# Optimization experiments

Measured on AMD Instinct MI355X. Metric: run time of the kernel, lower is better.

Reference implementation:

```python
import jax, jax.numpy as jnp
import numpy as np

CH = 512
COND = 1280
HEADS = 8
GROUPS = CH // 8
EPS = 1e-5


def conv2d(x, w, b, pad):
    y = jax.lax.conv_general_dilated(
        x, w, window_strides=(1, 1), padding=[(pad, pad), (pad, pad)],
        dimension_numbers=('NCHW', 'OIHW', 'NCHW'))
    return y + b[None, :, None, None]


def group_norm(x, gamma, beta, groups, eps=EPS):
    b, c, h, w = x.shape
    xg = x.reshape(b, groups, c // groups, h, w)
    mu = xg.mean(axis=(2, 3, 4), keepdims=True)
    var = xg.var(axis=(2, 3, 4), keepdims=True)
    xn = ((xg - mu) * jax.lax.rsqrt(var + eps)).reshape(b, c, h, w)
    return xn * gamma[None, :, None, None] + beta[None, :, None, None]


def setup_inputs() -> dict:
    key = jax.random.key(0)
    ks = jax.random.split(key, 20)
    s = 0.05
    inp = {
        'x': jax.random.normal(ks[0], (8, CH, 32, 32), jnp.float32),
        'conditioning': jax.random.normal(ks[1], (8, COND), jnp.float32),
        # ResBlock params
        'c1w': jax.random.normal(ks[2], (CH, CH, 3, 3), jnp.float32) * s,
        'c1b': jnp.zeros((CH,), jnp.float32),
        'g1w': jnp.ones((CH,), jnp.float32),
        'g1b': jnp.zeros((CH,), jnp.float32),
        'c2w': jax.random.normal(ks[3], (CH, CH, 3, 3), jnp.float32) * s,
        'c2b': jnp.zeros((CH,), jnp.float32),
        'g2w': jnp.ones((CH,), jnp.float32),
        'g2b': jnp.zeros((CH,), jnp.float32),
        'cpw': jax.random.normal(ks[4], (CH, COND), jnp.float32) * s,
        'cpb': jnp.zeros((CH,), jnp.float32),
        'rpw': jax.random.normal(ks[5], (CH, CH, 1, 1), jnp.float32) * s,
        'rpb': jnp.zeros((CH,), jnp.float32),
        # Attention params (1x1 convs)
        'qw': jax.random.normal(ks[6], (CH, CH, 1, 1), jnp.float32) * s,
        'qb': jnp.zeros((CH,), jnp.float32),
        'kw': jax.random.normal(ks[7], (CH, CH, 1, 1), jnp.float32) * s,
        'kb': jnp.zeros((CH,), jnp.float32),
        'vw': jax.random.normal(ks[8], (CH, CH, 1, 1), jnp.float32) * s,
        'vb': jnp.zeros((CH,), jnp.float32),
        'ow': jax.random.normal(ks[9], (CH, CH, 1, 1), jnp.float32) * s,
        'ob': jnp.zeros((CH,), jnp.float32),
    }
    return inp


def reference(x, conditioning, c1w, c1b, g1w, g1b, c2w, c2b, g2w, g2b,
              cpw, cpb, rpw, rpb, qw, qb, kw, kb, vw, vb, ow, ob):
    # --- ResBlock ---
    residual = conv2d(x, rpw, rpb, 0)
    h = conv2d(x, c1w, c1b, 1)
    h = group_norm(h, g1w, g1b, GROUPS)
    h = jax.nn.silu(h)
    h = conv2d(h, c2w, c2b, 1)
    h = group_norm(h, g2w, g2b, GROUPS)
    cond = conditioning @ cpw.T + cpb  # [B, C]
    h = h * (1.0 + cond[:, :, None, None]) + residual

    # --- SpatialSelfAttention ---
    b, c, hh, ww = h.shape
    d = c // HEADS
    scale = d ** (-0.5)
    q = conv2d(h, qw, qb, 0).reshape(b, HEADS, d, hh * ww)
    k = conv2d(h, kw, kb, 0).reshape(b, HEADS, d, hh * ww)
    v = conv2d(h, vw, vb, 0).reshape(b, HEADS, d, hh * ww)
    attn = jnp.einsum('bhdn,bhdm->bhnm', q, k) * scale  # [B,H,N,N]
    attn = jax.nn.softmax(attn, axis=-1)
    out = jnp.einsum('bhnm,bhdm->bhdn', attn, v).reshape(b, c, hh, ww)
    return conv2d(out, ow, ob, 0) + h
```

## Files before the change

### kernel.cpp

```cpp
#include <hip/hip_runtime.h>
#include <hip/hip_bf16.h>

typedef unsigned short u16;
typedef unsigned long long u64;
typedef __attribute__((ext_vector_type(8))) short bf8;
typedef __attribute__((ext_vector_type(4))) short bf4;
typedef __attribute__((ext_vector_type(4))) float f32x4;

#define CH_ 512
#define NSP 1024
#define NB 8
#define CONDDIM 1280
#define NGROUP 64
#define HEADS_ 8
#define HD 64
#define PR 34
#define PPB (PR*PR)
#define QSCALE 0.18033688011112042f

#define VWAIT(N) asm volatile("s_waitcnt vmcnt(" #N ")" ::: "memory")
#define SCHEDB __builtin_amdgcn_sched_barrier(0)
#define BARRIER do { SCHEDB; __builtin_amdgcn_s_barrier(); SCHEDB; } while (0)

__device__ __forceinline__ u16 f2bf(float f) {
  union { float f; unsigned u; } v; v.f = f;
  unsigned u = v.u;
  return (u16)((u + 0x7fffu + ((u >> 16) & 1u)) >> 16);
}

__device__ __forceinline__ unsigned cvt_pk_bf16(float lo, float hi) {
  unsigned r;
  asm volatile("v_cvt_pk_bf16_f32 %0, %1, %2" : "=v"(r) : "v"(lo), "v"(hi));
  return r;
}

__device__ __forceinline__ f32x4 mfma_bf16(bf8 a, bf8 b, f32x4 c) {
  return __builtin_amdgcn_mfma_f32_16x16x32_bf16(a, b, c, 0, 0, 0);
}

__device__ __forceinline__ void gload16(const void* g, void* l) {
  __builtin_amdgcn_global_load_lds((const __attribute__((address_space(1))) void*)g,
                                   (__attribute__((address_space(3))) void*)l, 16, 0, 0);
}


__global__ __launch_bounds__(1024) void pack_x_kernel(const float* __restrict__ x, u16* __restrict__ xp) {
  __shared__ float t[32][33];
  int b = blockIdx.z;
  int c0 = blockIdx.y * 32, p0 = blockIdx.x * 32;
  int tx = threadIdx.x & 31, ty = threadIdx.x >> 5;
  t[ty][tx] = x[((size_t)b * CH_ + c0 + ty) * NSP + p0 + tx];
  __syncthreads();
  int p = p0 + ty;
  int y = p >> 5, xc = p & 31;
  xp[((size_t)b * PPB + (size_t)(y + 1) * PR + xc + 1) * CH_ + c0 + tx] = f2bf(t[tx][ty]);
}

__global__ __launch_bounds__(256) void border_zero_kernel(u16* __restrict__ a, u16* __restrict__ b) {
  int id = blockIdx.x * 256 + threadIdx.x;
  if (id >= NB * 132 * 64) return;
  int ch8 = id & 63;
  int rest = id >> 6;
  int bidx = rest % 132;
  int bb = rest / 132;
  int r, c;
  if (bidx < 34)       { r = 0;          c = bidx; }
  else if (bidx < 68)  { r = 33;         c = bidx - 34; }
  else if (bidx < 100) { r = bidx - 67;  c = 0; }
  else                 { r = bidx - 99;  c = 33; }
  size_t off = ((size_t)bb * PPB + (size_t)r * PR + c) * CH_ + ch8 * 8;
  const bf8 z = {0, 0, 0, 0, 0, 0, 0, 0};
  *(bf8*)(a + off) = z;
  *(bf8*)(b + off) = z;
}

__global__ __launch_bounds__(256) void pack_w3_kernel(const float* __restrict__ wA, const float* __restrict__ wB,
                                                      u16* __restrict__ dA, u16* __restrict__ dB) {
  int id = blockIdx.x * 256 + threadIdx.x;
  if (id >= 9 * 64 * CH_) return;
  const float* w = blockIdx.y ? wB : wA;
  u16* wp = blockIdx.y ? dB : dA;
  int co = id & (CH_ - 1);
  int cib = (id >> 9) & 63;
  int t = id >> 15;
  int dy = t / 3, dx = t % 3;
  bf8 v;
#pragma unroll
  for (int j = 0; j < 8; j++) {
    int ci = cib * 8 + j;
    v[j] = (short)f2bf(w[(((size_t)co * CH_ + ci) * 3 + dy) * 3 + dx]);
  }
  *(bf8*)(wp + ((size_t)(t * 64 + cib) * CH_ + co) * 8) = v;
}

__global__ __launch_bounds__(256) void pack_w1_kernel(
    const float* __restrict__ s0, const float* __restrict__ s1, const float* __restrict__ s2,
    const float* __restrict__ s3, const float* __restrict__ s4,
    u16* __restrict__ d0, u16* __restrict__ d1, u16* __restrict__ d2,
    u16* __restrict__ d3, u16* __restrict__ d4) {
  int id = blockIdx.x * 256 + threadIdx.x;
  if (id >= 64 * CH_) return;
  const float* w; u16* wp;
  switch (blockIdx.y) {
    case 0: w = s0; wp = d0; break;
    case 1: w = s1; wp = d1; break;
    case 2: w = s2; wp = d2; break;
    case 3: w = s3; wp = d3; break;
    default: w = s4; wp = d4; break;
  }
  int co = id & (CH_ - 1);
  int cib = id >> 9;
  bf8 v;
#pragma unroll
  for (int j = 0; j < 8; j++) v[j] = (short)f2bf(w[(size_t)co * CH_ + cib * 8 + j]);
  *(bf8*)(wp + ((size_t)cib * CH_ + co) * 8) = v;
}

__global__ __launch_bounds__(256) void cond_kernel(const float* __restrict__ cd, const float* __restrict__ cpw,
                                                   const float* __restrict__ cpb, float* __restrict__ cond) {
  int b = blockIdx.y;
  int c = blockIdx.x * 4 + (threadIdx.x >> 6);
  int lane = threadIdx.x & 63;
  const float* wrow = cpw + (size_t)c * CONDDIM;
  const float* crow = cd + (size_t)b * CONDDIM;
  float s = 0.f;
  for (int i = lane; i < CONDDIM; i += 64) s += crow[i] * wrow[i];
#pragma unroll
  for (int m = 32; m > 0; m >>= 1) s += __shfl_xor(s, m, 64);
  if (lane == 0) cond[b * CH_ + c] = s + cpb[c];
}

template <int TAPS, int PIN, int EPI>
__global__ __launch_bounds__(256, 3) void conv_kernel(
    const u16* __restrict__ in, const u16* __restrict__ wp, const float* __restrict__ bias,
    float* __restrict__ outf, const float* __restrict__ addf,
    u16* __restrict__ o0, u16* __restrict__ o1, u16* __restrict__ o2,
    const float* __restrict__ b0, const float* __restrict__ b1, const float* __restrict__ b2) {
  constexpr int LDSZ = (TAPS == 9) ? (2 * 14336 + 2 * 12288) : (4 * 8192 + 4 * 4096);
  __shared__ char lds[LDSZ];
  char* ldsA = lds;
  char* ldsB = lds + ((TAPS == 9) ? 2 * 14336 : 4 * 8192);

  const int b = blockIdx.z;
  int seg = 0, coy = blockIdx.y;
  if constexpr (EPI == 5) { seg = coy >> 3; coy &= 7; }
  const int co0 = coy * 64;
  const int p0 = blockIdx.x * 128;
  const int tid = threadIdx.x;
  const int lane = tid & 63, wid = tid >> 6;
  const int wv = wid >> 1, wc = wid & 1;
  const int l15 = lane & 15, lhi = lane >> 4;

  const char* aSrc;
  if constexpr (TAPS == 9) {
    aSrc = (const char*)in + ((size_t)b * PPB + (size_t)blockIdx.x * 4 * PR) * 1024;
  } else if constexpr (PIN) {
    aSrc = (const char*)in + (size_t)b * PPB * 1024;
  } else {
    aSrc = (const char*)in + ((size_t)b * NSP + p0) * 1024;
  }
  const char* bSrc = (const char*)wp + (size_t)((EPI == 5) ? seg * 524288 : 0) + co0 * 16;

  const int pB = ((tid >> 6) * 512 + (tid & 63)) * 16;
  int pA0, pA1, pA3 = 0;
  if constexpr (TAPS == 9) {
    pA0 = ((tid >> 2) << 10) + ((tid & 3) << 4);
    pA3 = ((192 + ((tid & 127) >> 2)) << 10) + ((tid & 3) << 4);
    pA1 = 0;
  } else {
    int a0 = (tid >> 2), a1 = 64 + (tid >> 2);
    if constexpr (PIN) {
      int pp0 = p0 + a0, pp1 = p0 + a1;
      int g0 = ((pp0 >> 5) + 1) * PR + (pp0 & 31) + 1;
      int g1 = ((pp1 >> 5) + 1) * PR + (pp1 & 31) + 1;
      pA0 = (g0 << 10) + ((tid & 3) << 4);
      pA1 = (g1 << 10) + ((tid & 3) << 4);
    } else {
      pA0 = (a0 << 10) + ((tid & 3) << 4);
      pA1 = (a1 << 10) + ((tid & 3) << 4);
    }
  }

  const int aAddr = (TAPS == 9) ? ((wv * 68 + l15) * 64 + lhi * 16)
                                : ((wv * 64 + l15) * 64 + lhi * 16);
  const int bAddr = (lhi * 64 + wc * 32 + l15) * 16;

  f32x4 acc[4][2];
#pragma unroll
  for (int m = 0; m < 4; m++)
#pragma unroll
    for (int n = 0; n < 2; n++) acc[m][n] = {0.f, 0.f, 0.f, 0.f};

  if constexpr (TAPS == 9) {
    gload16(aSrc + pA0,          ldsA + (wid << 10));
    gload16(aSrc + pA0 + 65536,  ldsA + 4096 + (wid << 10));
    gload16(aSrc + pA0 + 131072, ldsA + 8192 + (wid << 10));
    gload16(aSrc + pA3,          ldsA + 12288 + ((wid & 1) << 10));
    gload16(bSrc + pB,           ldsB + (wid << 10));
    gload16(bSrc + 524288 + pB,  ldsB + 4096 + (wid << 10));
    gload16(bSrc + 1048576 + pB, ldsB + 8192 + (wid << 10));
    VWAIT(0);
    BARRIER;

#define PH3(KC, T, AS, H) do {                                                          \
    const int kcn_ = ((KC) < 15) ? (KC) + 1 : 15;                                       \
    { const int kb_ = ((T) == 2) ? kcn_ : (KC);                                         \
      const int tn_ = 3 * (((T) + 1) % 3);                                              \
      gload16(bSrc + (size_t)((tn_ + 0) * 64 + kb_ * 4) * 8192 + pB,                    \
              ldsB + (1 - (H)) * 12288 + (wid << 10));                                  \
      gload16(bSrc + (size_t)((tn_ + 1) * 64 + kb_ * 4) * 8192 + pB,                    \
              ldsB + (1 - (H)) * 12288 + 4096 + (wid << 10));                           \
      gload16(bSrc + (size_t)((tn_ + 2) * 64 + kb_ * 4) * 8192 + pB,                    \
              ldsB + (1 - (H)) * 12288 + 8192 + (wid << 10)); }                         \
    if constexpr ((T) == 0) {                                                           \
      gload16(aSrc + kcn_ * 64 + pA0,         ldsA + (1-(AS))*14336 + (wid << 10));     \
      gload16(aSrc + kcn_ * 64 + pA0 + 65536, ldsA + (1-(AS))*14336 + 4096 + (wid<<10));\
    }                                                                                   \
    if constexpr ((T) == 1)                                                             \
      gload16(aSrc + kcn_ * 64 + pA0 + 131072, ldsA + (1-(AS))*14336 + 8192 + (wid<<10));\
    if constexpr ((T) == 2)                                                             \
      gload16(aSrc + kcn_ * 64 + pA3, ldsA + (1-(AS))*14336 + 12288 + ((wid&1)<<10));   \
    SCHEDB;                                                                             \
    {                                                                                   \
      const char* Ab_ = ldsA + (AS) * 14336;                                            \
      const char* Bb_ = ldsB + (H) * 12288;                                             \
      bf8 af_[3][4], bq_[3][2];                                                         \
      _Pragma("unroll")                                                                 \
      for (int tt = 0; tt < 3; tt++) {                                                  \
        const int DT_ = (T) * 34 + tt;                                                  \
        af_[tt][0] = *(const bf8*)(Ab_ + DT_ * 64 + 0    + aAddr);                      \
        af_[tt][1] = *(const bf8*)(Ab_ + DT_ * 64 + 1024 + aAddr);                      \
        af_[tt][2] = *(const bf8*)(Ab_ + DT_ * 64 + 2176 + aAddr);                      \
        af_[tt][3] = *(const bf8*)(Ab_ + DT_ * 64 + 3200 + aAddr);                      \
        bq_[tt][0] = *(const bf8*)(Bb_ + tt * 4096 + 0   + bAddr);                      \
        bq_[tt][1] = *(const bf8*)(Bb_ + tt * 4096 + 256 + bAddr);                      \
      }                                                                                 \
      __builtin_amdgcn_s_setprio(1);                                                    \
      _Pragma("unroll")                                                                 \
      for (int tt = 0; tt < 3; tt++)                                                    \
        _Pragma("unroll")                                                               \
        for (int m = 0; m < 4; m++) {                                                   \
          acc[m][0] = mfma_bf16(af_[tt][m], bq_[tt][0], acc[m][0]);                     \
          acc[m][1] = mfma_bf16(af_[tt][m], bq_[tt][1], acc[m][1]);                     \
        }                                                                               \
      __builtin_amdgcn_s_setprio(0);                                                    \
    }                                                                                   \
    if constexpr ((T) == 0) { VWAIT(2); } else if constexpr ((T) == 1) { VWAIT(1); }    \
    else { VWAIT(0); }                                                                  \
    BARRIER;                                                                            \
  } while (0)

    for (int kc2 = 0; kc2 < 8; kc2++) {
      PH3(kc2 * 2,     0, 0, 0); PH3(kc2 * 2,     1, 0, 1); PH3(kc2 * 2,     2, 0, 0);
      PH3(kc2 * 2 + 1, 0, 1, 1); PH3(kc2 * 2 + 1, 1, 1, 0); PH3(kc2 * 2 + 1, 2, 1, 1);
    }
#undef PH3
  } else {
    gload16(aSrc + pA0,         ldsA + (wid << 10));
    gload16(aSrc + pA1,         ldsA + 4096 + (wid << 10));
    gload16(bSrc + pB,          ldsB + (wid << 10));
    gload16(aSrc + 64 + pA0,    ldsA + 8192 + (wid << 10));
    gload16(aSrc + 64 + pA1,    ldsA + 8192 + 4096 + (wid << 10));
    gload16(bSrc + 32768 + pB,  ldsB + 4096 + (wid << 10));
    VWAIT(3);
    BARRIER;

#define PH1(KC, S) do {                                                                 \
    constexpr int S2 = ((S) + 2) & 3;                                                   \
    const int kcn_ = ((KC) + 2 < 16) ? (KC) + 2 : 15;                                   \
    gload16(bSrc + (size_t)kcn_ * 32768 + pB, ldsB + S2 * 4096 + (wid << 10));          \
    gload16(aSrc + kcn_ * 64 + pA0, ldsA + S2 * 8192 + (wid << 10));                    \
    gload16(aSrc + kcn_ * 64 + pA1, ldsA + S2 * 8192 + 4096 + (wid << 10));             \
    SCHEDB;                                                                             \
    bf8 af0 = *(const bf8*)(ldsA + (S) * 8192 + 0    + aAddr);                          \
    bf8 af1 = *(const bf8*)(ldsA + (S) * 8192 + 1024 + aAddr);                          \
    bf8 af2 = *(const bf8*)(ldsA + (S) * 8192 + 2048 + aAddr);                          \
    bf8 af3 = *(const bf8*)(ldsA + (S) * 8192 + 3072 + aAddr);                          \
    bf8 bq0 = *(const bf8*)(ldsB + (S) * 4096 + 0   + bAddr);                           \
    bf8 bq1 = *(const bf8*)(ldsB + (S) * 4096 + 256 + bAddr);                           \
    __builtin_amdgcn_s_setprio(1);                                                      \
    acc[0][0] = mfma_bf16(af0, bq0, acc[0][0]);                                         \
    acc[0][1] = mfma_bf16(af0, bq1, acc[0][1]);                                         \
    acc[1][0] = mfma_bf16(af1, bq0, acc[1][0]);                                         \
    acc[1][1] = mfma_bf16(af1, bq1, acc[1][1]);                                         \
    acc[2][0] = mfma_bf16(af2, bq0, acc[2][0]);                                         \
    acc[2][1] = mfma_bf16(af2, bq1, acc[2][1]);                                         \
    acc[3][0] = mfma_bf16(af3, bq0, acc[3][0]);                                         \
    acc[3][1] = mfma_bf16(af3, bq1, acc[3][1]);                                         \
    __builtin_amdgcn_s_setprio(0);                                                      \
    VWAIT(3);                                                                           \
    BARRIER;                                                                            \
  } while (0)

    for (int kc4 = 0; kc4 < 4; kc4++) {
      PH1(kc4 * 4 + 0, 0); PH1(kc4 * 4 + 1, 1); PH1(kc4 * 4 + 2, 2); PH1(kc4 * 4 + 3, 3);
    }
#undef PH1
  }

  VWAIT(0);

#pragma unroll
  for (int m = 0; m < 4; m++) {
    int pbase = p0 + wv * 64 + m * 16 + lhi * 4;
#pragma unroll
    for (int n = 0; n < 2; n++) {
      int co = co0 + wc * 32 + n * 16 + l15;
      if constexpr (EPI == 0) {
        float bv = bias[co];
#pragma unroll
        for (int r = 0; r < 4; r++)
          outf[((size_t)b * NSP + pbase + r) * CH_ + co] = acc[m][n][r] + bv;
      } else if constexpr (EPI == 2) {
        float bv = bias[co];
        f32x4 v;
#pragma unroll
        for (int r = 0; r < 4; r++)
          v[r] = acc[m][n][r] + bv + addf[((size_t)b * NSP + pbase + r) * CH_ + co];
        *(f32x4*)(outf + ((size_t)b * CH_ + co) * NSP + pbase) = v;
      } else {
        if (seg == 0) {
          float bv = b0[co];
#pragma unroll
          for (int r = 0; r < 4; r++)
            o0[((size_t)b * NSP + pbase + r) * CH_ + co] = f2bf((acc[m][n][r] + bv) * QSCALE);
        } else if (seg == 1) {
          float bv = b1[co];
#pragma unroll
          for (int r = 0; r < 4; r++)
            o1[((size_t)b * NSP + pbase + r) * CH_ + co] = f2bf(acc[m][n][r] + bv);
        } else {
          float bv = b2[co];
          union { bf4 v; u64 u; } pk4;
#pragma unroll
          for (int r = 0; r < 4; r++) pk4.v[r] = (short)f2bf(acc[m][n][r] + bv);
          int np = (pbase & ~31) | ((pbase & 12) << 1) | ((pbase & 16) >> 2);
          *(u64*)(o2 + ((size_t)b * CH_ + co) * NSP + np) = pk4.u;
        }
      }
    }
  }
}

template <int MODE>
__global__ __launch_bounds__(256) void gn_kernel(
    const float* __restrict__ in, const float* __restrict__ gw, const float* __restrict__ gb,
    const float* __restrict__ cond, const float* __restrict__ resid,
    float* __restrict__ outf, u16* __restrict__ outb) {
  int b = blockIdx.y, g = blockIdx.x;
  int tid = threadIdx.x;
  int c = g * 8 + (tid & 7);
  int prow = tid >> 3;
  const float* base = in + (size_t)b * NSP * CH_ + c;
  float v[32];
  float s = 0.f, ss = 0.f;
#pragma unroll
  for (int i = 0; i < 32; i++) {
    v[i] = base[(size_t)(prow + i * 32) * CH_];
    s += v[i]; ss += v[i] * v[i];
  }
  __shared__ float rs[256], rss[256];
  rs[tid] = s; rss[tid] = ss;
  __syncthreads();
  for (int off = 128; off > 0; off >>= 1) {
    if (tid < off) { rs[tid] += rs[tid + off]; rss[tid] += rss[tid + off]; }
    __syncthreads();
  }
  float mean = rs[0] * (1.f / 8192.f);
  float var = rss[0] * (1.f / 8192.f) - mean * mean;
  float inv = rsqrtf(var + 1e-5f);
  float gamma = gw[c], beta = gb[c];
  float cm = 0.f;
  if (MODE == 1) cm = 1.f + cond[b * CH_ + c];
#pragma unroll
  for (int i = 0; i < 32; i++) {
    int p = prow + i * 32;
    float y = (v[i] - mean) * inv * gamma + beta;
    if (MODE == 0) {
      float sg = 1.f / (1.f + __expf(-y));
      int yy = p >> 5, xc = p & 31;
      outb[((size_t)b * PPB + (size_t)(yy + 1) * PR + xc + 1) * CH_ + c] = f2bf(y * sg);
    } else {
      size_t idx = ((size_t)b * NSP + p) * CH_ + c;
      float z = y * cm + resid[idx];
      outf[idx] = z;
      outb[idx] = f2bf(z);
    }
  }
}

__global__ __launch_bounds__(256, 2) void attn_kernel(const u16* __restrict__ q, const u16* __restrict__ k,
                                                      const u16* __restrict__ vT, u16* __restrict__ ao) {
  int bid = blockIdx.x;
  int swz = (bid & 7) * 64 + (bid >> 3);
  int b = swz >> 6;
  int head = (swz >> 3) & 7;
  int qt = swz & 7;
  int tid = threadIdx.x, lane = tid & 63, wid = tid >> 6;
  int l15 = lane & 15, lhi = lane >> 4;
  int cb = head * HD;
  int q0 = qt * 128 + wid * 32;

  const char* qp = (const char*)(q + (size_t)b * NSP * CH_ + cb);
  const char* kp = (const char*)(k + (size_t)b * NSP * CH_ + cb);
  const char* vp = (const char*)(vT + ((size_t)b * CH_ + cb) * NSP);

  __shared__ u16 Ksh[3][64 * 64];
  __shared__ u16 Vsh[3][64 * 64];

  bf8 aq[2][2];
#pragma unroll
  for (int qh = 0; qh < 2; qh++)
#pragma unroll
    for (int ks = 0; ks < 2; ks++)
      aq[qh][ks] = *(const bf8*)(qp + ((size_t)(q0 + qh * 16 + l15) * CH_ + ks * 32 + lhi * 8) * 2);

  const bf8 ones8 = {16256, 16256, 16256, 16256, 16256, 16256, 16256, 16256};

  f32x4 o[2][4], osum[2];
#pragma unroll
  for (int qh = 0; qh < 2; qh++) {
    osum[qh] = {0.f, 0.f, 0.f, 0.f};
#pragma unroll
    for (int n = 0; n < 4; n++) o[qh][n] = {0.f, 0.f, 0.f, 0.f};
  }

  auto stage = [&](int kt, int buf) {
#pragma unroll
    for (int t = 0; t < 2; t++) {
      int i = wid * 2 + t;
      int chunk = i * 64 + lane;
      int r = chunk >> 3, c = chunk & 7;
      gload16(kp + (size_t)(kt * 64 + r) * 1024 + (size_t)((c ^ (r & 7)) * 16),
              (char*)Ksh[buf] + i * 1024);
    }
#pragma unroll
    for (int t = 0; t < 2; t++) {
      int i = wid * 2 + t;
      int chunk = i * 64 + lane;
      int r = chunk >> 3, c = chunk & 7;
      gload16(vp + (size_t)r * 2048 + (size_t)(kt * 128) + (size_t)((c ^ (r & 7)) * 16),
              (char*)Vsh[buf] + i * 1024);
    }
  };

  auto qk = [&](int buf, f32x4 (&sacc)[2][4]) {
    const char* Kb = (const char*)Ksh[0] + buf * 8192;
#pragma unroll
    for (int qh = 0; qh < 2; qh++)
#pragma unroll
      for (int kf = 0; kf < 4; kf++) sacc[qh][kf] = {0.f, 0.f, 0.f, 0.f};
#pragma unroll
    for (int kf = 0; kf < 4; kf++) {
      bf8 ak[2];
#pragma unroll
      for (int ks = 0; ks < 2; ks++)
        ak[ks] = *(const bf8*)(Kb + (size_t)(kf * 16 + l15) * 128 + (((ks * 4 + lhi) ^ (l15 & 7)) * 16));
#pragma unroll
      for (int qh = 0; qh < 2; qh++)
#pragma unroll
        for (int ks = 0; ks < 2; ks++)
          sacc[qh][kf] = mfma_bf16(ak[ks], aq[qh][ks], sacc[qh][kf]);
    }
  };

  auto smpv = [&](int buf, f32x4 (&sacc)[2][4]) {
    const char* Vb = (const char*)Vsh[0] + buf * 8192;
    unsigned pk[2][4][2];
#pragma unroll
    for (int qh = 0; qh < 2; qh++)
#pragma unroll
      for (int kf = 0; kf < 4; kf++) {
        f32x4 pv;
#pragma unroll
        for (int r = 0; r < 4; r++) pv[r] = exp2f(sacc[qh][kf][r]);
        pk[qh][kf][0] = cvt_pk_bf16(pv[0], pv[1]);
        pk[qh][kf][1] = cvt_pk_bf16(pv[2], pv[3]);
      }
#pragma unroll
    for (int g = 0; g < 2; g++) {
      union { bf8 v8; unsigned u[4]; } ap[2];
#pragma unroll
      for (int qh = 0; qh < 2; qh++) {
        ap[qh].u[0] = pk[qh][2 * g][0];
        ap[qh].u[1] = pk[qh][2 * g][1];
        ap[qh].u[2] = pk[qh][2 * g + 1][0];
        ap[qh].u[3] = pk[qh][2 * g + 1][1];
      }
#pragma unroll
      for (int nf2 = 0; nf2 < 4; nf2++) {
        int row = nf2 * 16 + l15;
        bf8 bv8 = *(const bf8*)(Vb + (size_t)row * 128 + (((4 * g + lhi) ^ (l15 & 7)) * 16));
#pragma unroll
        for (int qh = 0; qh < 2; qh++)
          o[qh][nf2] = mfma_bf16(ap[qh].v8, bv8, o[qh][nf2]);
      }
#pragma unroll
      for (int qh = 0; qh < 2; qh++)
        osum[qh] = mfma_bf16(ap[qh].v8, ones8, osum[qh]);
    }
  };

  stage(0, 0);
  stage(1, 1);
  VWAIT(4);
  BARRIER;

  f32x4 saccA[2][4], saccB[2][4];
  qk(0, saccA);

  int bc = 0;
  for (int kt2 = 0; kt2 < 8; kt2++) {
    {
      int kt = 2 * kt2;
      int bn = (bc == 2) ? 0 : bc + 1;
      int bs = (bn == 2) ? 0 : bn + 1;
      VWAIT(0);
      BARRIER;
      qk(bn, saccB);
      if (kt < 14) stage(kt + 2, bs);
      smpv(bc, saccA);
      bc = bn;
    }
    {
      int kt = 2 * kt2 + 1;
      if (kt < 15) {
        int bn = (bc == 2) ? 0 : bc + 1;
        int bs = (bn == 2) ? 0 : bn + 1;
        VWAIT(0);
        BARRIER;
        qk(bn, saccA);
        if (kt < 14) stage(kt + 2, bs);
        smpv(bc, saccB);
        bc = bn;
      } else {
        smpv(bc, saccB);
      }
    }
  }

#pragma unroll
  for (int qh = 0; qh < 2; qh++) {
    float linv[4];
#pragma unroll
    for (int r = 0; r < 4; r++) linv[r] = 1.f / osum[qh][r];
#pragma unroll
    for (int nf2 = 0; nf2 < 4; nf2++)
#pragma unroll
      for (int r = 0; r < 4; r++) {
        float val = o[qh][nf2][r] * linv[r];
        ao[((size_t)b * NSP + q0 + qh * 16 + lhi * 4 + r) * CH_ + cb + nf2 * 16 + l15] = f2bf(val);
      }
  }
}


extern "C" void kernel_launch(void* const* d_in, const int* in_sizes, int n_in,
                              void* d_out, int out_size, void* d_ws, size_t ws_size,
                              hipStream_t stream) {
  const float* x    = (const float*)d_in[0];
  const float* cnd  = (const float*)d_in[1];
  const float* c1w  = (const float*)d_in[2];
  const float* c1b  = (const float*)d_in[3];
  const float* g1w  = (const float*)d_in[4];
  const float* g1b  = (const float*)d_in[5];
  const float* c2w  = (const float*)d_in[6];
  const float* c2b  = (const float*)d_in[7];
  const float* g2w  = (const float*)d_in[8];
  const float* g2b  = (const float*)d_in[9];
  const float* cpw  = (const float*)d_in[10];
  const float* cpb  = (const float*)d_in[11];
  const float* rpw  = (const float*)d_in[12];
  const float* rpb  = (const float*)d_in[13];
  const float* qw   = (const float*)d_in[14];
  const float* qb   = (const float*)d_in[15];
  const float* kw   = (const float*)d_in[16];
  const float* kb   = (const float*)d_in[17];
  const float* vw   = (const float*)d_in[18];
  const float* vb   = (const float*)d_in[19];
  const float* ow   = (const float*)d_in[20];
  const float* ob   = (const float*)d_in[21];
  float* out = (float*)d_out;

  char* ws = (char*)d_ws;
  size_t off = 0;
  auto alloc = [&](size_t bytes) -> char* {
    char* p = ws + off;
    off = (off + bytes + 255) & ~(size_t)255;
    return p;
  };
  const size_t ACT_F = (size_t)NB * NSP * CH_ * 4;
  const size_t ACT_B = (size_t)NB * NSP * CH_ * 2;
  const size_t PAD_B = (size_t)NB * PPB * CH_ * 2;

  u16* xp    = (u16*)alloc(PAD_B);
  u16* h1p   = (u16*)alloc(PAD_B);
  u16* w1p   = (u16*)alloc((size_t)9 * CH_ * CH_ * 2);
  u16* w2p   = (u16*)alloc((size_t)9 * CH_ * CH_ * 2);
  u16* wrp   = (u16*)alloc((size_t)CH_ * CH_ * 2);
  u16* wqkv  = (u16*)alloc((size_t)3 * CH_ * CH_ * 2);
  u16* wop   = (u16*)alloc((size_t)CH_ * CH_ * 2);
  float* cndv = (float*)alloc((size_t)NB * CH_ * 4);
  float* resid = (float*)alloc(ACT_F);
  float* h12  = (float*)alloc(ACT_F);
  u16* hb    = (u16*)alloc(ACT_B);
  u16* qbuf  = (u16*)alloc(ACT_B);
  u16* kbuf  = (u16*)alloc(ACT_B);
  u16* vTb   = (u16*)alloc(ACT_B);
  u16* aob   = (u16*)alloc(ACT_B);
  if (off > ws_size) return;

  dim3 tgrid(NSP / 32, CH_ / 32, NB);
  border_zero_kernel<<<(NB * 132 * 64 + 255) / 256, 256, 0, stream>>>(xp, h1p);
  pack_x_kernel<<<tgrid, 1024, 0, stream>>>(x, xp);
  pack_w3_kernel<<<dim3((9 * 64 * CH_ + 255) / 256, 2), 256, 0, stream>>>(c1w, c2w, w1p, w2p);
  pack_w1_kernel<<<dim3((64 * CH_) / 256, 5), 256, 0, stream>>>(
      rpw, qw, kw, vw, ow,
      wrp, wqkv, wqkv + (size_t)CH_ * CH_, wqkv + (size_t)2 * CH_ * CH_, wop);
  cond_kernel<<<dim3(CH_ / 4, NB), 256, 0, stream>>>(cnd, cpw, cpb, cndv);

  dim3 ggrid(NSP / 128, CH_ / 64, NB);
  dim3 qgrid(NSP / 128, 3 * CH_ / 64, NB);
  conv_kernel<9, 1, 0><<<ggrid, 256, 0, stream>>>(xp, w1p, c1b, h12, nullptr,
                                                  nullptr, nullptr, nullptr, nullptr, nullptr, nullptr);
  conv_kernel<1, 1, 0><<<ggrid, 256, 0, stream>>>(xp, wrp, rpb, resid, nullptr,
                                                  nullptr, nullptr, nullptr, nullptr, nullptr, nullptr);
  gn_kernel<0><<<dim3(NGROUP, NB), 256, 0, stream>>>(h12, g1w, g1b, nullptr, nullptr, nullptr, h1p);
  conv_kernel<9, 1, 0><<<ggrid, 256, 0, stream>>>(h1p, w2p, c2b, h12, nullptr,
                                                  nullptr, nullptr, nullptr, nullptr, nullptr, nullptr);
  gn_kernel<1><<<dim3(NGROUP, NB), 256, 0, stream>>>(h12, g2w, g2b, cndv, resid, h12, hb);
  conv_kernel<1, 0, 5><<<qgrid, 256, 0, stream>>>(hb, wqkv, nullptr, nullptr, nullptr,
                                                  qbuf, kbuf, vTb, qb, kb, vb);
  attn_kernel<<<512, 256, 0, stream>>>(qbuf, kbuf, vTb, aob);
  conv_kernel<1, 0, 2><<<ggrid, 256, 0, stream>>>(aob, wop, ob, out, h12,
                                                  nullptr, nullptr, nullptr, nullptr, nullptr, nullptr);
}
```

Before: 246.5 us.

## Fuse residual 1x1 conv into first 3x3 conv and triple-buffer weight tiles

The residual 1x1 projection is folded into the first 3x3 conv kernel. Its weights are loaded into an extra LDS region and multiplied against the already-loaded center-tap A fragments, so the separate residual conv launch and its reread of x go away. The weight pipeline also changes from double buffering to three per-tap-row buffers, with deeper vmcnt waits. In exchange the kernel uses more LDS and accumulator registers, which may reduce occupancy under the launch bound of 3.

```diff
diff --git a/kernel.cpp b/kernel.cpp
--- a/kernel.cpp
+++ b/kernel.cpp
@@ -135,11 +135,14 @@
     const u16* __restrict__ in, const u16* __restrict__ wp, const float* __restrict__ bias,
     float* __restrict__ outf, const float* __restrict__ addf,
     u16* __restrict__ o0, u16* __restrict__ o1, u16* __restrict__ o2,
-    const float* __restrict__ b0, const float* __restrict__ b1, const float* __restrict__ b2) {
-  constexpr int LDSZ = (TAPS == 9) ? (2 * 14336 + 2 * 12288) : (4 * 8192 + 4 * 4096);
+    const float* __restrict__ b0, const float* __restrict__ b1, const float* __restrict__ b2,
+    const u16* __restrict__ wp2, float* __restrict__ outf2, const float* __restrict__ bias2) {
+  constexpr int LDSZ = (TAPS == 9) ? (2 * 14336 + 3 * 12288 + (EPI == 6 ? 2 * 4096 : 0))
+                                   : (4 * 8192 + 4 * 4096);
   __shared__ char lds[LDSZ];
   char* ldsA = lds;
   char* ldsB = lds + ((TAPS == 9) ? 2 * 14336 : 4 * 8192);
+  char* ldsR = lds + 2 * 14336 + 3 * 12288;
 
   const int b = blockIdx.z;
   int seg = 0, coy = blockIdx.y;
@@ -160,6 +163,7 @@
     aSrc = (const char*)in + ((size_t)b * NSP + p0) * 1024;
   }
   const char* bSrc = (const char*)wp + (size_t)((EPI == 5) ? seg * 524288 : 0) + co0 * 16;
+  const char* rSrc = (const char*)wp2 + co0 * 16;
 
   const int pB = ((tid >> 6) * 512 + (tid & 63)) * 16;
   int pA0, pA1, pA3 = 0;
@@ -185,45 +189,57 @@
                                 : ((wv * 64 + l15) * 64 + lhi * 16);
   const int bAddr = (lhi * 64 + wc * 32 + l15) * 16;
 
-  f32x4 acc[4][2];
+  f32x4 acc[4][2], accR[4][2];
 #pragma unroll
   for (int m = 0; m < 4; m++)
 #pragma unroll
-    for (int n = 0; n < 2; n++) acc[m][n] = {0.f, 0.f, 0.f, 0.f};
+    for (int n = 0; n < 2; n++) { acc[m][n] = {0.f, 0.f, 0.f, 0.f}; accR[m][n] = {0.f, 0.f, 0.f, 0.f}; }
 
   if constexpr (TAPS == 9) {
     gload16(aSrc + pA0,          ldsA + (wid << 10));
     gload16(aSrc + pA0 + 65536,  ldsA + 4096 + (wid << 10));
     gload16(aSrc + pA0 + 131072, ldsA + 8192 + (wid << 10));
     gload16(aSrc + pA3,          ldsA + 12288 + ((wid & 1) << 10));
-    gload16(bSrc + pB,           ldsB + (wid << 10));
-    gload16(bSrc + 524288 + pB,  ldsB + 4096 + (wid << 10));
-    gload16(bSrc + 1048576 + pB, ldsB + 8192 + (wid << 10));
-    VWAIT(0);
+    gload16(bSrc + (size_t)(0 * 64) * 8192 + pB, ldsB + (wid << 10));
+    gload16(bSrc + (size_t)(1 * 64) * 8192 + pB, ldsB + 4096 + (wid << 10));
+    gload16(bSrc + (size_t)(2 * 64) * 8192 + pB, ldsB + 8192 + (wid << 10));
+    gload16(bSrc + (size_t)(3 * 64) * 8192 + pB, ldsB + 12288 + (wid << 10));
+    gload16(bSrc + (size_t)(4 * 64) * 8192 + pB, ldsB + 12288 + 4096 + (wid << 10));
+    gload16(bSrc + (size_t)(5 * 64) * 8192 + pB, ldsB + 12288 + 8192 + (wid << 10));
+    if constexpr (EPI == 6) {
+      gload16(rSrc + pB, ldsR + (wid << 10));
+      VWAIT(4);
+    } else {
+      VWAIT(3);
+    }
     BARRIER;
 
-#define PH3(KC, T, AS, H) do {                                                          \
+#define PH3(KC, T, AS) do {                                                             \
     const int kcn_ = ((KC) < 15) ? (KC) + 1 : 15;                                       \
-    { const int kb_ = ((T) == 2) ? kcn_ : (KC);                                         \
-      const int tn_ = 3 * (((T) + 1) % 3);                                              \
-      gload16(bSrc + (size_t)((tn_ + 0) * 64 + kb_ * 4) * 8192 + pB,                    \
-              ldsB + (1 - (H)) * 12288 + (wid << 10));                                  \
-      gload16(bSrc + (size_t)((tn_ + 1) * 64 + kb_ * 4) * 8192 + pB,                    \
-              ldsB + (1 - (H)) * 12288 + 4096 + (wid << 10));                           \
-      gload16(bSrc + (size_t)((tn_ + 2) * 64 + kb_ * 4) * 8192 + pB,                    \
-              ldsB + (1 - (H)) * 12288 + 8192 + (wid << 10)); }                         \
     if constexpr ((T) == 0) {                                                           \
-      gload16(aSrc + kcn_ * 64 + pA0,         ldsA + (1-(AS))*14336 + (wid << 10));     \
-      gload16(aSrc + kcn_ * 64 + pA0 + 65536, ldsA + (1-(AS))*14336 + 4096 + (wid<<10));\
+      gload16(bSrc + (size_t)(6 * 64 + (KC) * 4) * 8192 + pB, ldsB + 24576 + (wid << 10)); \
+      gload16(bSrc + (size_t)(7 * 64 + (KC) * 4) * 8192 + pB, ldsB + 24576 + 4096 + (wid << 10)); \
+      gload16(bSrc + (size_t)(8 * 64 + (KC) * 4) * 8192 + pB, ldsB + 24576 + 8192 + (wid << 10)); \
+      gload16(aSrc + kcn_ * 64 + pA0,         ldsA + (1 - (AS)) * 14336 + (wid << 10)); \
+      gload16(aSrc + kcn_ * 64 + pA0 + 65536, ldsA + (1 - (AS)) * 14336 + 4096 + (wid << 10)); \
+    } else if constexpr ((T) == 1) {                                                    \
+      gload16(bSrc + (size_t)(0 * 64 + kcn_ * 4) * 8192 + pB, ldsB + (wid << 10));      \
+      gload16(bSrc + (size_t)(1 * 64 + kcn_ * 4) * 8192 + pB, ldsB + 4096 + (wid << 10)); \
+      gload16(bSrc + (size_t)(2 * 64 + kcn_ * 4) * 8192 + pB, ldsB + 8192 + (wid << 10)); \
+      gload16(aSrc + kcn_ * 64 + pA0 + 131072, ldsA + (1 - (AS)) * 14336 + 8192 + (wid << 10)); \
+      if constexpr (EPI == 6)                                                           \
+        if ((KC) < 15)                                                                  \
+          gload16(rSrc + (size_t)kcn_ * 32768 + pB, ldsR + (kcn_ & 1) * 4096 + (wid << 10)); \
+    } else {                                                                            \
+      gload16(bSrc + (size_t)(3 * 64 + kcn_ * 4) * 8192 + pB, ldsB + 12288 + (wid << 10)); \
+      gload16(bSrc + (size_t)(4 * 64 + kcn_ * 4) * 8192 + pB, ldsB + 12288 + 4096 + (wid << 10)); \
+      gload16(bSrc + (size_t)(5 * 64 + kcn_ * 4) * 8192 + pB, ldsB + 12288 + 8192 + (wid << 10)); \
+      gload16(aSrc + kcn_ * 64 + pA3, ldsA + (1 - (AS)) * 14336 + 12288 + ((wid & 1) << 10)); \
     }                                                                                   \
-    if constexpr ((T) == 1)                                                             \
-      gload16(aSrc + kcn_ * 64 + pA0 + 131072, ldsA + (1-(AS))*14336 + 8192 + (wid<<10));\
-    if constexpr ((T) == 2)                                                             \
-      gload16(aSrc + kcn_ * 64 + pA3, ldsA + (1-(AS))*14336 + 12288 + ((wid&1)<<10));   \
     SCHEDB;                                                                             \
     {                                                                                   \
       const char* Ab_ = ldsA + (AS) * 14336;                                            \
-      const char* Bb_ = ldsB + (H) * 12288;                                             \
+      const char* Bb_ = ldsB + (T) * 12288;                                             \
       bf8 af_[3][4], bq_[3][2];                                                         \
       _Pragma("unroll")                                                                 \
       for (int tt = 0; tt < 3; tt++) {                                                  \
@@ -243,16 +259,27 @@
           acc[m][0] = mfma_bf16(af_[tt][m], bq_[tt][0], acc[m][0]);                     \
           acc[m][1] = mfma_bf16(af_[tt][m], bq_[tt][1], acc[m][1]);                     \
         }                                                                               \
+      if constexpr (EPI == 6 && (T) == 1) {                                             \
+        bf8 rq0 = *(const bf8*)(ldsR + ((KC) & 1) * 4096 + 0   + bAddr);                \
+        bf8 rq1 = *(const bf8*)(ldsR + ((KC) & 1) * 4096 + 256 + bAddr);                \
+        _Pragma("unroll")                                                               \
+        for (int m = 0; m < 4; m++) {                                                   \
+          accR[m][0] = mfma_bf16(af_[1][m], rq0, accR[m][0]);                           \
+          accR[m][1] = mfma_bf16(af_[1][m], rq1, accR[m][1]);                           \
+        }                                                                               \
+      }                                                                                 \
       __builtin_amdgcn_s_setprio(0);                                                    \
     }                                                                                   \
-    if constexpr ((T) == 0) { VWAIT(2); } else if constexpr ((T) == 1) { VWAIT(1); }    \
-    else { VWAIT(0); }                                                                  \
+    if constexpr ((T) == 0) { VWAIT(5); }                                               \
+    else if constexpr ((T) == 1) {                                                      \
+      if constexpr (EPI == 6) { VWAIT(5); } else { VWAIT(4); }                          \
+    } else { VWAIT(4); }                                                                \
     BARRIER;                                                                            \
   } while (0)
 
     for (int kc2 = 0; kc2 < 8; kc2++) {
-      PH3(kc2 * 2,     0, 0, 0); PH3(kc2 * 2,     1, 0, 1); PH3(kc2 * 2,     2, 0, 0);
-      PH3(kc2 * 2 + 1, 0, 1, 1); PH3(kc2 * 2 + 1, 1, 1, 0); PH3(kc2 * 2 + 1, 2, 1, 1);
+      PH3(kc2 * 2,     0, 0); PH3(kc2 * 2,     1, 0); PH3(kc2 * 2,     2, 0);
+      PH3(kc2 * 2 + 1, 0, 1); PH3(kc2 * 2 + 1, 1, 1); PH3(kc2 * 2 + 1, 2, 1);
     }
 #undef PH3
   } else {
@@ -311,6 +338,15 @@
 #pragma unroll
         for (int r = 0; r < 4; r++)
           outf[((size_t)b * NSP + pbase + r) * CH_ + co] = acc[m][n][r] + bv;
+      } else if constexpr (EPI == 6) {
+        float bv = bias[co];
+        float rv = bias2[co];
+#pragma unroll
+        for (int r = 0; r < 4; r++) {
+          size_t idx = ((size_t)b * NSP + pbase + r) * CH_ + co;
+          outf[idx]  = acc[m][n][r] + bv;
+          outf2[idx] = accR[m][n][r] + rv;
+        }
       } else if constexpr (EPI == 2) {
         float bv = bias[co];
         f32x4 v;
@@ -621,17 +657,19 @@
 
   dim3 ggrid(NSP / 128, CH_ / 64, NB);
   dim3 qgrid(NSP / 128, 3 * CH_ / 64, NB);
-  conv_kernel<9, 1, 0><<<ggrid, 256, 0, stream>>>(xp, w1p, c1b, h12, nullptr,
-                                                  nullptr, nullptr, nullptr, nullptr, nullptr, nullptr);
-  conv_kernel<1, 1, 0><<<ggrid, 256, 0, stream>>>(xp, wrp, rpb, resid, nullptr,
-                                                  nullptr, nullptr, nullptr, nullptr, nullptr, nullptr);
+  conv_kernel<9, 1, 6><<<ggrid, 256, 0, stream>>>(xp, w1p, c1b, h12, nullptr,
+                                                  nullptr, nullptr, nullptr, nullptr, nullptr, nullptr,
+                                                  wrp, resid, rpb);
   gn_kernel<0><<<dim3(NGROUP, NB), 256, 0, stream>>>(h12, g1w, g1b, nullptr, nullptr, nullptr, h1p);
   conv_kernel<9, 1, 0><<<ggrid, 256, 0, stream>>>(h1p, w2p, c2b, h12, nullptr,
-                                                  nullptr, nullptr, nullptr, nullptr, nullptr, nullptr);
+                                                  nullptr, nullptr, nullptr, nullptr, nullptr, nullptr,
+                                                  nullptr, nullptr, nullptr);
   gn_kernel<1><<<dim3(NGROUP, NB), 256, 0, stream>>>(h12, g2w, g2b, cndv, resid, h12, hb);
   conv_kernel<1, 0, 5><<<qgrid, 256, 0, stream>>>(hb, wqkv, nullptr, nullptr, nullptr,
-                                                  qbuf, kbuf, vTb, qb, kb, vb);
+                                                  qbuf, kbuf, vTb, qb, kb, vb,
+                                                  nullptr, nullptr, nullptr);
   attn_kernel<<<512, 256, 0, stream>>>(qbuf, kbuf, vTb, aob);
   conv_kernel<1, 0, 2><<<ggrid, 256, 0, stream>>>(aob, wop, ob, out, h12,
-                                                  nullptr, nullptr, nullptr, nullptr, nullptr, nullptr);
-}
+                                                  nullptr, nullptr, nullptr, nullptr, nullptr, nullptr,
+                                                  nullptr, nullptr, nullptr);
+}
```

Result: faster. 238.2 us (-3.4%).
